# Kernel tuning notes

Hardware: AMD Instinct MI355X
Metric: run time of the kernel (lower is better)

Reference implementation:

```python
import jax, jax.numpy as jnp
import numpy as np

HEADS = 16
DIMS = [64, 64, 64, 64]  # [d_att(Q), d_att(K), d_ff(V), d_ff(G)]
EPS = 1e-4
P_POW = 2


def _cdist(Q, K):
    # Euclidean pairwise distance via the norm expansion, like torch.cdist.
    # Q: [h, b, t, d], K: [h, b, t, d] -> [h, b, t, t]
    q2 = jnp.sum(Q * Q, axis=-1)  # [h, b, t]
    k2 = jnp.sum(K * K, axis=-1)  # [h, b, t]
    qk = jnp.einsum('hbtd,hbsd->hbts', Q, K)
    d2 = q2[..., :, None] + k2[..., None, :] - 2.0 * qk
    return jnp.sqrt(jnp.maximum(d2, 0.0))


def setup_inputs() -> dict:
    key = jax.random.key(0)
    ks = jax.random.split(key, 4)
    b, t, d_in = 2, 2048, 1024
    d_proj = HEADS * sum(DIMS)  # 4096
    X = jax.random.normal(ks[0], (b, t, d_in), dtype=jnp.float32)
    W_in = jax.random.normal(ks[1], (d_in, d_proj), dtype=jnp.float32) * (d_in ** -0.5)
    b_in = jnp.zeros((d_proj,), dtype=jnp.float32)
    W_out = jax.random.normal(ks[2], (HEADS * DIMS[2], d_in), dtype=jnp.float32) * ((HEADS * DIMS[2]) ** -0.5)
    b_out = jnp.zeros((d_in,), dtype=jnp.float32)
    return {"X": X, "W_in": W_in, "b_in": b_in, "W_out": W_out, "b_out": b_out}


def reference(X, W_in, b_in, W_out, b_out):
    b, t, _ = X.shape
    # multi-head input projection: [b,t,d_in] -> [h,b,t,sum(DIMS)] -> split
    P = X @ W_in + b_in                       # [b, t, h*sum(DIMS)]
    P = P.reshape(b, t, HEADS, sum(DIMS))
    P = jnp.transpose(P, (2, 0, 1, 3))        # [h, b, t, sum(DIMS)]
    splits = np.cumsum(DIMS)[:-1]
    Q, K, V, G = jnp.split(P, splits, axis=-1)
    # Shepard's attention: inverse-power-distance weights
    W = jnp.power(EPS + _cdist(Q, K), -P_POW)         # [h, b, t, t]
    W = W / (EPS + jnp.sum(W, axis=-1, keepdims=True))
    A = jnp.einsum('hbts,hbse->hbte', W, V)           # [h, b, t, e]
    H = G * A                                          # gating
    H = jnp.transpose(H, (1, 2, 0, 3)).reshape(b, t, HEADS * DIMS[2])
    return H @ W_out + b_out
```

## Files before the change

### kernel.cpp

```cpp
#include <hip/hip_runtime.h>
#include <hip/hip_bf16.h>
#include <cstdint>
#include <cstddef>

typedef __bf16 bf16_t;
typedef __attribute__((ext_vector_type(8))) __bf16 bf16x8;
typedef __attribute__((ext_vector_type(4))) float f32x4;
typedef __attribute__((ext_vector_type(16))) float f32x16;
typedef __attribute__((ext_vector_type(4))) unsigned int u32x4;

#define ATT_EPS 1e-4f

__device__ __forceinline__ f32x4 mfma_bf16(bf16x8 a, bf16x8 b, f32x4 c) {
  return __builtin_amdgcn_mfma_f32_16x16x32_bf16(a, b, c, 0, 0, 0);
}
__device__ __forceinline__ f32x16 mfma32(bf16x8 a, bf16x8 b, f32x16 c) {
  return __builtin_amdgcn_mfma_f32_32x32x16_bf16(a, b, c, 0, 0, 0);
}
__device__ __forceinline__ unsigned cvtpk_bf16(float lo, float hi) {
  unsigned r;
  asm("v_cvt_pk_bf16_f32 %0, %1, %2" : "=v"(r) : "v"(lo), "v"(hi));
  return r;
}

#define GLDS16(g, l)                                                          \
  __builtin_amdgcn_global_load_lds(                                           \
      (const __attribute__((address_space(1))) void*)(g),                     \
      (__attribute__((address_space(3))) void*)(l), 16, 0, 0)

__global__ __launch_bounds__(256) void cvt_x_kernel(
    const float* __restrict__ X, bf16_t* __restrict__ Xb, int n8) {
  int i = blockIdx.x * 256 + threadIdx.x;
  if (i >= n8) return;
  f32x4 a = ((const f32x4*)X)[i * 2 + 0];
  f32x4 b = ((const f32x4*)X)[i * 2 + 1];
  bf16x8 o;
  o[0] = (__bf16)a[0]; o[1] = (__bf16)a[1]; o[2] = (__bf16)a[2]; o[3] = (__bf16)a[3];
  o[4] = (__bf16)b[0]; o[5] = (__bf16)b[1]; o[6] = (__bf16)b[2]; o[7] = (__bf16)b[3];
  ((bf16x8*)Xb)[i] = o;
}

__global__ __launch_bounds__(256) void tcvt_kernel(
    const float* __restrict__ W, bf16_t* __restrict__ Wt, int R, int C) {
  __shared__ float T[64][65];
  int tx = threadIdx.x & 63, ty = threadIdx.x >> 6;
  int c0 = blockIdx.x * 64, r0 = blockIdx.y * 64;
#pragma unroll
  for (int i = 0; i < 16; ++i) {
    int rr = ty * 16 + i;
    T[rr][tx] = W[(size_t)(r0 + rr) * C + c0 + tx];
  }
  __syncthreads();
#pragma unroll
  for (int i = 0; i < 16; ++i) {
    int cc = ty * 16 + i;
    Wt[(size_t)(c0 + cc) * R + r0 + tx] = (bf16_t)T[tx][cc];
  }
}

__global__ __launch_bounds__(256) void vt_kernel(
    const bf16_t* __restrict__ P, bf16_t* __restrict__ VtG) {
  __shared__ float T[64][65];
  int h = blockIdx.x;
  int r0 = blockIdx.y * 64;
  int tx = threadIdx.x & 63, ty = threadIdx.x >> 6;
  const bf16_t* src = P + (size_t)r0 * 4096 + h * 256 + 128;
#pragma unroll
  for (int i = 0; i < 16; ++i) {
    int rr = ty * 16 + i;
    T[rr][tx] = (float)src[(size_t)rr * 4096 + tx];
  }
  __syncthreads();
  int ptx = (tx & ~15) | ((tx & 3) | ((tx & 4) << 1) | ((tx & 8) >> 1));
#pragma unroll
  for (int i = 0; i < 16; ++i) {
    int cc = ty * 16 + i;
    VtG[(size_t)(h * 64 + cc) * 4096 + r0 + ptx] = (bf16_t)T[tx][cc];
  }
}

template <int OUTF32>
__global__ __launch_bounds__(256, 2) void gemm_kernel(
    const bf16_t* __restrict__ A, const bf16_t* __restrict__ Bt,
    const float* __restrict__ bias, void* __restrict__ Cout,
    int M, int N, int K) {
  __shared__ bf16_t As[2][128 * 64];
  __shared__ bf16_t Bs[2][128 * 64];
  int tid = threadIdx.x, lane = tid & 63, wv = tid >> 6;
  int l15 = lane & 15, lhi = lane >> 4;
  int NT = N >> 7;
  int nwg = gridDim.x;
  int qq = nwg >> 3;
  int swz = (blockIdx.x & 7) * qq + (blockIdx.x >> 3);
  int tm = swz / NT, tn = swz % NT;
  int m0 = tm << 7, n0 = tn << 7;
  int wm = (wv >> 1) << 6, wn = (wv & 1) << 6;
  int KT = K >> 6;

  auto stage = [&](int buf, int kt) {
    int k0 = kt << 6;
#pragma unroll
    for (int s = 0; s < 4; ++s) {
      int t = s * 256 + tid;
      int row = t >> 3, u = t & 7;
      int cc = (u ^ (row & 7)) << 3;
      GLDS16(A + (size_t)(m0 + row) * K + k0 + cc, &As[buf][t * 8]);
    }
#pragma unroll
    for (int s = 0; s < 4; ++s) {
      int t = s * 256 + tid;
      int row = t >> 3, u = t & 7;
      int cc = (u ^ (row & 7)) << 3;
      GLDS16(Bt + (size_t)(n0 + row) * K + k0 + cc, &Bs[buf][t * 8]);
    }
  };

  f32x4 zero = {0.f, 0.f, 0.f, 0.f};
  f32x4 acc[4][4];
#pragma unroll
  for (int ms = 0; ms < 4; ++ms)
#pragma unroll
    for (int ns = 0; ns < 4; ++ns) acc[ms][ns] = zero;

  stage(0, 0);
  __syncthreads();
  int cur = 0;
  for (int kt = 0; kt < KT; ++kt) {
    if (kt + 1 < KT) stage(cur ^ 1, kt + 1);
#pragma unroll
    for (int ks = 0; ks < 2; ++ks) {
      bf16x8 af[4], bfr[4];
#pragma unroll
      for (int ms = 0; ms < 4; ++ms) {
        int row = wm + ms * 16 + l15;
        af[ms] = *(const bf16x8*)&As[cur][row * 64 + (((ks * 4 + lhi) ^ (row & 7)) << 3)];
      }
#pragma unroll
      for (int ns = 0; ns < 4; ++ns) {
        int col = wn + ns * 16 + l15;
        bfr[ns] = *(const bf16x8*)&Bs[cur][col * 64 + (((ks * 4 + lhi) ^ (col & 7)) << 3)];
      }
#pragma unroll
      for (int ms = 0; ms < 4; ++ms)
#pragma unroll
        for (int ns = 0; ns < 4; ++ns)
          acc[ms][ns] = mfma_bf16(af[ms], bfr[ns], acc[ms][ns]);
    }
    __syncthreads();
    cur ^= 1;
  }

#pragma unroll
  for (int ns = 0; ns < 4; ++ns) {
    int col = n0 + wn + ns * 16 + l15;
    float bv = bias[col];
#pragma unroll
    for (int ms = 0; ms < 4; ++ms) {
      int rowb = m0 + wm + ms * 16 + lhi * 4;
#pragma unroll
      for (int r = 0; r < 4; ++r) {
        float v = acc[ms][ns][r] + bv;
        if (OUTF32)
          ((float*)Cout)[(size_t)(rowb + r) * N + col] = v;
        else
          ((bf16_t*)Cout)[(size_t)(rowb + r) * N + col] = (bf16_t)v;
      }
    }
  }
}

__global__ __launch_bounds__(256) void norms_kernel(
    const bf16_t* __restrict__ P, float* __restrict__ Q2, bf16_t* __restrict__ K2E) {
  int tid = threadIdx.x, lane = tid & 63, wv = tid >> 6;
  int wg = blockIdx.x * 4 + wv;
  int h = wg >> 9, rb = wg & 511;
  int r = rb * 8 + (lane >> 3), ch = lane & 7;
  const bf16_t* base = P + (size_t)r * 4096 + h * 256 + ch * 8;
  bf16x8 qv = *(const bf16x8*)base;
  bf16x8 kv = *(const bf16x8*)(base + 64);
  float sq = 0.f, sk = 0.f;
#pragma unroll
  for (int j = 0; j < 8; ++j) {
    float a = (float)qv[j];
    sq += a * a;
    float c = (float)kv[j];
    sk += c * c;
  }
#pragma unroll
  for (int m = 1; m <= 4; m <<= 1) {
    sq += __shfl_xor(sq, m);
    sk += __shfl_xor(sk, m);
  }
  if (ch == 0) {
    Q2[h * 4096 + r] = sq;
    __bf16 kh = (__bf16)sk;
    __bf16 kl = (__bf16)(sk - (float)kh);
    bf16x8 row;
    row[0] = kh; row[1] = kl;
    row[2] = (__bf16)1.f; row[3] = (__bf16)1.f;
    row[4] = (__bf16)0.f; row[5] = (__bf16)0.f;
    row[6] = (__bf16)0.f; row[7] = (__bf16)0.f;
    *(bf16x8*)&K2E[((size_t)h * 4096 + r) * 8] = row;
  }
}

__global__ __launch_bounds__(512, 4) void attn_kernel(
    const bf16_t* __restrict__ P, const bf16_t* __restrict__ VtG,
    const float* __restrict__ Q2, const bf16_t* __restrict__ K2E,
    bf16_t* __restrict__ H) {
  __shared__ union Smem {
    struct {
      bf16_t Ks[2][128 * 64];
      bf16_t Vts[2][64 * 128];
      bf16_t K2e[2][128 * 8];
    } l;
    float Comb[4][64][33];
  } sm;
  __shared__ float invLds[4][32];

  int tid = threadIdx.x, lane = tid & 63, wv = tid >> 6;
  int l31 = lane & 31, hi = lane >> 5, hi4 = hi * 4;
  int qw = wv & 3, sw = wv >> 2;
  int sOff = sw * 64;
  int swz = (blockIdx.x & 7) * 64 + (blockIdx.x >> 3);
  int hb = swz >> 4, qt = swz & 15;
  int h = hb >> 1, b = hb & 1;
  int rowbase = b * 2048;
  const bf16_t* Pq = P + (size_t)rowbase * 4096 + h * 256;
  const bf16_t* Pk = Pq + 64;
  const bf16_t* Pg = Pq + 192;
  const bf16_t* Vg = VtG + (size_t)h * 64 * 4096 + rowbase;
  const float* Q2g = Q2 + h * 4096 + rowbase;
  const bf16_t* K2Eg = K2E + ((size_t)h * 4096 + rowbase) * 8;
  int q0 = qt * 128 + qw * 32;

  auto stageKV = [&](int buf, int s0) {
#pragma unroll
    for (int s4 = 0; s4 < 2; ++s4) {
      int t = s4 * 512 + tid;
      int row = t >> 3, u = t & 7;
      int cc = (u ^ (row & 7)) << 3;
      GLDS16(Pk + (size_t)(s0 + row) * 4096 + cc, &sm.l.Ks[buf][t * 8]);
    }
#pragma unroll
    for (int s4 = 0; s4 < 2; ++s4) {
      int t = s4 * 512 + tid;
      int row = t >> 4, u = t & 15;
      int cc = (u ^ (row & 7)) << 3;
      GLDS16(Vg + (size_t)row * 4096 + s0 + cc, &sm.l.Vts[buf][t * 8]);
    }
    if (tid < 128)
      GLDS16(K2Eg + (size_t)(s0 + tid) * 8, &sm.l.K2e[buf][tid * 8]);
  };

  bf16x8 qm[4];
#pragma unroll
  for (int db = 0; db < 4; ++db) {
    bf16x8 q = *(const bf16x8*)(Pq + (size_t)(q0 + l31) * 4096 + db * 16 + hi * 8);
    u32x4 u = *(u32x4*)&q;
    u = (u ^ 0x80008000u) + 0x00800080u;
    qm[db] = *(bf16x8*)&u;
  }
  float q2s = Q2g[q0 + l31];
  __bf16 q2h = (__bf16)q2s;
  __bf16 q2l = (__bf16)(q2s - (float)q2h);
  bf16x8 qmE;
  qmE[0] = hi ? (__bf16)0.f : (__bf16)1.f;
  qmE[1] = qmE[0];
  qmE[2] = hi ? (__bf16)0.f : q2h;
  qmE[3] = hi ? (__bf16)0.f : q2l;
  qmE[4] = (__bf16)0.f; qmE[5] = (__bf16)0.f;
  qmE[6] = (__bf16)0.f; qmE[7] = (__bf16)0.f;

  f32x16 zero16;
#pragma unroll
  for (int r = 0; r < 16; ++r) zero16[r] = 0.f;

  f32x16 nacc0, nacc1;
#pragma unroll
  for (int r = 0; r < 16; ++r) { nacc0[r] = 0.f; nacc1[r] = 0.f; }
  float dacc0 = 0.f, dacc1 = 0.f;

  stageKV(0, 0);
  __syncthreads();

  for (int st = 0; st < 16; ++st) {
    int cur = st & 1;
    int s0 = st * 128;
    if (st + 1 < 16) stageKV(cur ^ 1, s0 + 128);

    const bf16_t* KsC = sm.l.Ks[cur];
    const bf16_t* VtC = sm.l.Vts[cur];
    const bf16_t* K2eC = sm.l.K2e[cur];
#pragma unroll
    for (int sb = 0; sb < 2; ++sb) {
      int sbase = sOff + sb * 32;
      int srow = sbase + l31;
      bf16x8 ke = *(const bf16x8*)&K2eC[srow * 8];
      u32x4 keu = *(u32x4*)&ke;
      u32x4 kz;
      kz[0] = hi ? 0u : keu[0];
      kz[1] = hi ? 0u : keu[1];
      kz[2] = 0u; kz[3] = 0u;
      bf16x8 kfE = *(bf16x8*)&kz;
      f32x16 D = mfma32(kfE, qmE, zero16);
#pragma unroll
      for (int db = 0; db < 4; ++db) {
        bf16x8 kf = *(const bf16x8*)&KsC[srow * 64 + (((db * 2 + hi) ^ (srow & 7)) << 3)];
        D = mfma32(kf, qm[db], D);
      }
      float p[16];
#pragma unroll
      for (int r = 0; r < 16; ++r) {
        float w = __builtin_amdgcn_rcpf(fmaxf(D[r], 1e-12f));
        if (r & 1) dacc1 += w; else dacc0 += w;
        p[r] = w;
      }
      u32x4 w0v = {cvtpk_bf16(p[0], p[1]), cvtpk_bf16(p[2], p[3]),
                   cvtpk_bf16(p[4], p[5]), cvtpk_bf16(p[6], p[7])};
      u32x4 w1v = {cvtpk_bf16(p[8], p[9]), cvtpk_bf16(p[10], p[11]),
                   cvtpk_bf16(p[12], p[13]), cvtpk_bf16(p[14], p[15])};
      bf16x8 pa0 = *(bf16x8*)&w0v;
      bf16x8 pa1 = *(bf16x8*)&w1v;
      int e = l31;
      int ciB = (sOff >> 3) + sb * 4;
      bf16x8 vb00 = *(const bf16x8*)&VtC[e * 128 + (((ciB + 0 + hi) ^ (e & 7)) << 3)];
      bf16x8 vb01 = *(const bf16x8*)&VtC[(e + 32) * 128 + (((ciB + 0 + hi) ^ ((e + 32) & 7)) << 3)];
      bf16x8 vb10 = *(const bf16x8*)&VtC[e * 128 + (((ciB + 2 + hi) ^ (e & 7)) << 3)];
      bf16x8 vb11 = *(const bf16x8*)&VtC[(e + 32) * 128 + (((ciB + 2 + hi) ^ ((e + 32) & 7)) << 3)];
      nacc0 = mfma32(pa0, vb00, nacc0);
      nacc1 = mfma32(pa0, vb01, nacc1);
      nacc0 = mfma32(pa1, vb10, nacc0);
      nacc1 = mfma32(pa1, vb11, nacc1);
    }
    __syncthreads();
  }

  if (sw == 1) {
#pragma unroll
    for (int r = 0; r < 16; ++r) {
      sm.Comb[qw][lane][r] = nacc0[r];
      sm.Comb[qw][lane][16 + r] = nacc1[r];
    }
    sm.Comb[qw][lane][32] = dacc0 + dacc1;
  }
  __syncthreads();
  if (sw == 0) {
    float dacc = dacc0 + dacc1 + sm.Comb[qw][lane][32];
#pragma unroll
    for (int r = 0; r < 16; ++r) {
      nacc0[r] += sm.Comb[qw][lane][r];
      nacc1[r] += sm.Comb[qw][lane][16 + r];
    }
    dacc += __shfl_xor(dacc, 32);
    float inv = __builtin_amdgcn_rcpf(ATT_EPS + dacc);
    if (lane < 32) invLds[qw][l31] = inv;
    __builtin_amdgcn_s_waitcnt(0);
#pragma unroll
    for (int r = 0; r < 16; ++r) {
      int q = (r & 3) + 8 * (r >> 2) + hi4;
      int tq = q0 + q;
      float iv = invLds[qw][q];
      float g0 = (float)Pg[(size_t)tq * 4096 + l31];
      float g1 = (float)Pg[(size_t)tq * 4096 + 32 + l31];
      H[(size_t)(rowbase + tq) * 1024 + h * 64 + l31] = (bf16_t)(g0 * nacc0[r] * iv);
      H[(size_t)(rowbase + tq) * 1024 + h * 64 + 32 + l31] = (bf16_t)(g1 * nacc1[r] * iv);
    }
  }
}

extern "C" void kernel_launch(void* const* d_in, const int* in_sizes, int n_in,
                              void* d_out, int out_size, void* d_ws, size_t ws_size,
                              hipStream_t stream) {
  const float* X     = (const float*)d_in[0];
  const float* W_in  = (const float*)d_in[1];
  const float* b_in  = (const float*)d_in[2];
  const float* W_out = (const float*)d_in[3];
  const float* b_out = (const float*)d_in[4];

  char* ws = (char*)d_ws;
  bf16_t* Xb  = (bf16_t*)(ws);
  bf16_t* VtG = (bf16_t*)(ws);
  bf16_t* WbT = (bf16_t*)(ws + ((size_t)8  << 20));
  bf16_t* K2E = (bf16_t*)(ws + ((size_t)8  << 20));
  bf16_t* WoT = (bf16_t*)(ws + ((size_t)16 << 20));
  bf16_t* Pb  = (bf16_t*)(ws + ((size_t)18 << 20));
  bf16_t* Hb  = (bf16_t*)(ws + ((size_t)50 << 20));
  float*  Q2  = (float*) (ws + ((size_t)58 << 20));

  cvt_x_kernel<<<2048, 256, 0, stream>>>(X, Xb, 4096 * 1024 / 8);
  tcvt_kernel<<<dim3(64, 16), 256, 0, stream>>>(W_in, WbT, 1024, 4096);
  tcvt_kernel<<<dim3(16, 16), 256, 0, stream>>>(W_out, WoT, 1024, 1024);
  gemm_kernel<0><<<1024, 256, 0, stream>>>(Xb, WbT, b_in, Pb, 4096, 4096, 1024);
  norms_kernel<<<2048, 256, 0, stream>>>(Pb, Q2, K2E);
  vt_kernel<<<dim3(16, 64), 256, 0, stream>>>(Pb, VtG);
  attn_kernel<<<512, 512, 0, stream>>>(Pb, VtG, Q2, K2E, Hb);
  gemm_kernel<1><<<256, 256, 0, stream>>>(Hb, WoT, b_out, d_out, 4096, 1024, 1024);
}
```

Before: 137.0 us.

## Fuse norms and V transpose into projection GEMM epilogue; MFMA row-sum

The input-projection GEMM epilogue now computes the Q/K squared norms with lane shuffles. For V tiles it transposes through LDS and writes VtG directly, which removes the separate norms and vt kernels and their re-reads of P. V columns are no longer stored to P. The attention kernel computes the softmax denominator with an MFMA against a ones vector instead of scalar adds, and unrolls the K/V double buffer into explicit ping-pong stages. VtG and K2E now live in the output buffer as scratch, which is valid only because the final GEMM overwrites it afterwards.

```diff
diff --git a/kernel.cpp b/kernel.cpp
--- a/kernel.cpp
+++ b/kernel.cpp
@@ -58,32 +58,12 @@
   }
 }
 
-__global__ __launch_bounds__(256) void vt_kernel(
-    const bf16_t* __restrict__ P, bf16_t* __restrict__ VtG) {
-  __shared__ float T[64][65];
-  int h = blockIdx.x;
-  int r0 = blockIdx.y * 64;
-  int tx = threadIdx.x & 63, ty = threadIdx.x >> 6;
-  const bf16_t* src = P + (size_t)r0 * 4096 + h * 256 + 128;
-#pragma unroll
-  for (int i = 0; i < 16; ++i) {
-    int rr = ty * 16 + i;
-    T[rr][tx] = (float)src[(size_t)rr * 4096 + tx];
-  }
-  __syncthreads();
-  int ptx = (tx & ~15) | ((tx & 3) | ((tx & 4) << 1) | ((tx & 8) >> 1));
-#pragma unroll
-  for (int i = 0; i < 16; ++i) {
-    int cc = ty * 16 + i;
-    VtG[(size_t)(h * 64 + cc) * 4096 + r0 + ptx] = (bf16_t)T[tx][cc];
-  }
-}
-
-template <int OUTF32>
+template <int OUTF32, int FUSE>
 __global__ __launch_bounds__(256, 2) void gemm_kernel(
     const bf16_t* __restrict__ A, const bf16_t* __restrict__ Bt,
     const float* __restrict__ bias, void* __restrict__ Cout,
-    int M, int N, int K) {
+    int M, int N, int K,
+    float* __restrict__ Q2, bf16_t* __restrict__ K2E, bf16_t* __restrict__ VtG) {
   __shared__ bf16_t As[2][128 * 64];
   __shared__ bf16_t Bs[2][128 * 64];
   int tid = threadIdx.x, lane = tid & 63, wv = tid >> 6;
@@ -152,55 +132,87 @@
 
 #pragma unroll
   for (int ns = 0; ns < 4; ++ns) {
-    int col = n0 + wn + ns * 16 + l15;
-    float bv = bias[col];
-#pragma unroll
-    for (int ms = 0; ms < 4; ++ms) {
-      int rowb = m0 + wm + ms * 16 + lhi * 4;
-#pragma unroll
-      for (int r = 0; r < 4; ++r) {
-        float v = acc[ms][ns][r] + bv;
-        if (OUTF32)
-          ((float*)Cout)[(size_t)(rowb + r) * N + col] = v;
-        else
-          ((bf16_t*)Cout)[(size_t)(rowb + r) * N + col] = (bf16_t)v;
+    float bv = bias[n0 + wn + ns * 16 + l15];
+#pragma unroll
+    for (int ms = 0; ms < 4; ++ms)
+#pragma unroll
+      for (int r = 0; r < 4; ++r) acc[ms][ns][r] += bv;
+  }
+
+  bool vg = FUSE && ((n0 >> 7) & 1);
+  bool skipC = vg && (wn == 0);
+
+  if (!skipC) {
+#pragma unroll
+    for (int ns = 0; ns < 4; ++ns) {
+      int col = n0 + wn + ns * 16 + l15;
+#pragma unroll
+      for (int ms = 0; ms < 4; ++ms) {
+        int rowb = m0 + wm + ms * 16 + lhi * 4;
+#pragma unroll
+        for (int r = 0; r < 4; ++r) {
+          float v = acc[ms][ns][r];
+          if (OUTF32)
+            ((float*)Cout)[(size_t)(rowb + r) * N + col] = v;
+          else
+            ((bf16_t*)Cout)[(size_t)(rowb + r) * N + col] = (bf16_t)v;
+        }
       }
     }
   }
-}
-
-__global__ __launch_bounds__(256) void norms_kernel(
-    const bf16_t* __restrict__ P, float* __restrict__ Q2, bf16_t* __restrict__ K2E) {
-  int tid = threadIdx.x, lane = tid & 63, wv = tid >> 6;
-  int wg = blockIdx.x * 4 + wv;
-  int h = wg >> 9, rb = wg & 511;
-  int r = rb * 8 + (lane >> 3), ch = lane & 7;
-  const bf16_t* base = P + (size_t)r * 4096 + h * 256 + ch * 8;
-  bf16x8 qv = *(const bf16x8*)base;
-  bf16x8 kv = *(const bf16x8*)(base + 64);
-  float sq = 0.f, sk = 0.f;
-#pragma unroll
-  for (int j = 0; j < 8; ++j) {
-    float a = (float)qv[j];
-    sq += a * a;
-    float c = (float)kv[j];
-    sk += c * c;
-  }
-#pragma unroll
-  for (int m = 1; m <= 4; m <<= 1) {
-    sq += __shfl_xor(sq, m);
-    sk += __shfl_xor(sk, m);
-  }
-  if (ch == 0) {
-    Q2[h * 4096 + r] = sq;
-    __bf16 kh = (__bf16)sk;
-    __bf16 kl = (__bf16)(sk - (float)kh);
-    bf16x8 row;
-    row[0] = kh; row[1] = kl;
-    row[2] = (__bf16)1.f; row[3] = (__bf16)1.f;
-    row[4] = (__bf16)0.f; row[5] = (__bf16)0.f;
-    row[6] = (__bf16)0.f; row[7] = (__bf16)0.f;
-    *(bf16x8*)&K2E[((size_t)h * 4096 + r) * 8] = row;
+
+  if (FUSE) {
+    int h = n0 >> 8;
+    if (!vg) {
+#pragma unroll
+      for (int ms = 0; ms < 4; ++ms)
+#pragma unroll
+        for (int r = 0; r < 4; ++r) {
+          float s = 0.f;
+#pragma unroll
+          for (int ns = 0; ns < 4; ++ns) s += acc[ms][ns][r] * acc[ms][ns][r];
+          s += __shfl_xor(s, 1);
+          s += __shfl_xor(s, 2);
+          s += __shfl_xor(s, 4);
+          s += __shfl_xor(s, 8);
+          if (l15 == 0) {
+            int row = m0 + wm + ms * 16 + lhi * 4 + r;
+            if (wn == 0) {
+              Q2[h * 4096 + row] = s;
+            } else {
+              __bf16 kh = (__bf16)s;
+              __bf16 kl = (__bf16)(s - (float)kh);
+              bf16x8 rw;
+              rw[0] = kh; rw[1] = kl;
+              rw[2] = (__bf16)1.f; rw[3] = (__bf16)1.f;
+              rw[4] = (__bf16)0.f; rw[5] = (__bf16)0.f;
+              rw[6] = (__bf16)0.f; rw[7] = (__bf16)0.f;
+              *(bf16x8*)&K2E[((size_t)h * 4096 + row) * 8] = rw;
+            }
+          }
+        }
+    } else {
+      bf16_t* T = (bf16_t*)&As[0][0];
+      if (wn == 0) {
+#pragma unroll
+        for (int ms = 0; ms < 4; ++ms)
+#pragma unroll
+          for (int ns = 0; ns < 4; ++ns)
+#pragma unroll
+            for (int r = 0; r < 4; ++r) {
+              int row = wm + ms * 16 + lhi * 4 + r;
+              int e = ns * 16 + l15;
+              int prow = (row & ~15) | ((row & 3) | ((row & 4) << 1) | ((row & 8) >> 1));
+              T[e * 136 + prow] = (bf16_t)acc[ms][ns][r];
+            }
+      }
+      __syncthreads();
+      int e = tid >> 2, c0 = (tid & 3) * 32;
+      bf16_t* dst = VtG + (size_t)(h * 64 + e) * 4096 + m0 + c0;
+#pragma unroll
+      for (int j = 0; j < 4; ++j)
+        *(bf16x8*)&dst[j * 8] = *(bf16x8*)&T[e * 136 + c0 + j * 8];
+    }
   }
 }
 
@@ -214,9 +226,8 @@
       bf16_t Vts[2][64 * 128];
       bf16_t K2e[2][128 * 8];
     } l;
-    float Comb[4][64][33];
+    float Comb[4][64][49];
   } sm;
-  __shared__ float invLds[4][32];
 
   int tid = threadIdx.x, lane = tid & 63, wv = tid >> 6;
   int l31 = lane & 31, hi = lane >> 5, hi4 = hi * 4;
@@ -272,26 +283,20 @@
   qmE[4] = (__bf16)0.f; qmE[5] = (__bf16)0.f;
   qmE[6] = (__bf16)0.f; qmE[7] = (__bf16)0.f;
 
+  bf16x8 onesB;
+#pragma unroll
+  for (int j = 0; j < 8; ++j) onesB[j] = (__bf16)1.f;
+
   f32x16 zero16;
 #pragma unroll
   for (int r = 0; r < 16; ++r) zero16[r] = 0.f;
 
-  f32x16 nacc0, nacc1;
-#pragma unroll
-  for (int r = 0; r < 16; ++r) { nacc0[r] = 0.f; nacc1[r] = 0.f; }
-  float dacc0 = 0.f, dacc1 = 0.f;
-
-  stageKV(0, 0);
-  __syncthreads();
-
-  for (int st = 0; st < 16; ++st) {
-    int cur = st & 1;
-    int s0 = st * 128;
-    if (st + 1 < 16) stageKV(cur ^ 1, s0 + 128);
-
-    const bf16_t* KsC = sm.l.Ks[cur];
-    const bf16_t* VtC = sm.l.Vts[cur];
-    const bf16_t* K2eC = sm.l.K2e[cur];
+  f32x16 nacc0 = zero16, nacc1 = zero16, dvec = zero16;
+
+  auto compute = [&](int buf, int s0) {
+    const bf16_t* KsC = sm.l.Ks[buf];
+    const bf16_t* VtC = sm.l.Vts[buf];
+    const bf16_t* K2eC = sm.l.K2e[buf];
 #pragma unroll
     for (int sb = 0; sb < 2; ++sb) {
       int sbase = sOff + sb * 32;
@@ -311,17 +316,16 @@
       }
       float p[16];
 #pragma unroll
-      for (int r = 0; r < 16; ++r) {
-        float w = __builtin_amdgcn_rcpf(fmaxf(D[r], 1e-12f));
-        if (r & 1) dacc1 += w; else dacc0 += w;
-        p[r] = w;
-      }
+      for (int r = 0; r < 16; ++r)
+        p[r] = __builtin_amdgcn_rcpf(fmaxf(D[r], 1e-12f));
       u32x4 w0v = {cvtpk_bf16(p[0], p[1]), cvtpk_bf16(p[2], p[3]),
                    cvtpk_bf16(p[4], p[5]), cvtpk_bf16(p[6], p[7])};
       u32x4 w1v = {cvtpk_bf16(p[8], p[9]), cvtpk_bf16(p[10], p[11]),
                    cvtpk_bf16(p[12], p[13]), cvtpk_bf16(p[14], p[15])};
       bf16x8 pa0 = *(bf16x8*)&w0v;
       bf16x8 pa1 = *(bf16x8*)&w1v;
+      dvec = mfma32(pa0, onesB, dvec);
+      dvec = mfma32(pa1, onesB, dvec);
       int e = l31;
       int ciB = (sOff >> 3) + sb * 4;
       bf16x8 vb00 = *(const bf16x8*)&VtC[e * 128 + (((ciB + 0 + hi) ^ (e & 7)) << 3)];
@@ -333,6 +337,18 @@
       nacc0 = mfma32(pa1, vb10, nacc0);
       nacc1 = mfma32(pa1, vb11, nacc1);
     }
+  };
+
+  stageKV(0, 0);
+  __syncthreads();
+
+  for (int st2 = 0; st2 < 8; ++st2) {
+    int s0 = st2 * 256;
+    stageKV(1, s0 + 128);
+    compute(0, s0);
+    __syncthreads();
+    if (st2 < 7) stageKV(0, s0 + 256);
+    compute(1, s0 + 128);
     __syncthreads();
   }
 
@@ -341,26 +357,22 @@
     for (int r = 0; r < 16; ++r) {
       sm.Comb[qw][lane][r] = nacc0[r];
       sm.Comb[qw][lane][16 + r] = nacc1[r];
-    }
-    sm.Comb[qw][lane][32] = dacc0 + dacc1;
+      sm.Comb[qw][lane][32 + r] = dvec[r];
+    }
   }
   __syncthreads();
   if (sw == 0) {
-    float dacc = dacc0 + dacc1 + sm.Comb[qw][lane][32];
 #pragma unroll
     for (int r = 0; r < 16; ++r) {
       nacc0[r] += sm.Comb[qw][lane][r];
       nacc1[r] += sm.Comb[qw][lane][16 + r];
-    }
-    dacc += __shfl_xor(dacc, 32);
-    float inv = __builtin_amdgcn_rcpf(ATT_EPS + dacc);
-    if (lane < 32) invLds[qw][l31] = inv;
-    __builtin_amdgcn_s_waitcnt(0);
+      dvec[r] += sm.Comb[qw][lane][32 + r];
+    }
 #pragma unroll
     for (int r = 0; r < 16; ++r) {
       int q = (r & 3) + 8 * (r >> 2) + hi4;
       int tq = q0 + q;
-      float iv = invLds[qw][q];
+      float iv = __builtin_amdgcn_rcpf(ATT_EPS + dvec[r]);
       float g0 = (float)Pg[(size_t)tq * 4096 + l31];
       float g1 = (float)Pg[(size_t)tq * 4096 + 32 + l31];
       H[(size_t)(rowbase + tq) * 1024 + h * 64 + l31] = (bf16_t)(g0 * nacc0[r] * iv);
@@ -380,20 +392,20 @@
 
   char* ws = (char*)d_ws;
   bf16_t* Xb  = (bf16_t*)(ws);
-  bf16_t* VtG = (bf16_t*)(ws);
   bf16_t* WbT = (bf16_t*)(ws + ((size_t)8  << 20));
-  bf16_t* K2E = (bf16_t*)(ws + ((size_t)8  << 20));
   bf16_t* WoT = (bf16_t*)(ws + ((size_t)16 << 20));
   bf16_t* Pb  = (bf16_t*)(ws + ((size_t)18 << 20));
   bf16_t* Hb  = (bf16_t*)(ws + ((size_t)50 << 20));
   float*  Q2  = (float*) (ws + ((size_t)58 << 20));
+  bf16_t* VtG = (bf16_t*)d_out;
+  bf16_t* K2E = (bf16_t*)((char*)d_out + ((size_t)8 << 20));
 
   cvt_x_kernel<<<2048, 256, 0, stream>>>(X, Xb, 4096 * 1024 / 8);
   tcvt_kernel<<<dim3(64, 16), 256, 0, stream>>>(W_in, WbT, 1024, 4096);
   tcvt_kernel<<<dim3(16, 16), 256, 0, stream>>>(W_out, WoT, 1024, 1024);
-  gemm_kernel<0><<<1024, 256, 0, stream>>>(Xb, WbT, b_in, Pb, 4096, 4096, 1024);
-  norms_kernel<<<2048, 256, 0, stream>>>(Pb, Q2, K2E);
-  vt_kernel<<<dim3(16, 64), 256, 0, stream>>>(Pb, VtG);
+  gemm_kernel<0, 1><<<1024, 256, 0, stream>>>(Xb, WbT, b_in, Pb, 4096, 4096, 1024,
+                                              Q2, K2E, VtG);
   attn_kernel<<<512, 512, 0, stream>>>(Pb, VtG, Q2, K2E, Hb);
-  gemm_kernel<1><<<256, 256, 0, stream>>>(Hb, WoT, b_out, d_out, 4096, 1024, 1024);
-}
+  gemm_kernel<1, 0><<<256, 256, 0, stream>>>(Hb, WoT, b_out, d_out, 4096, 1024, 1024,
+                                             nullptr, nullptr, nullptr);
+}
```

Measured after the change: 141.8 us. +3.5%, slower.
